# Optimization experiments

Hardware: AMD Instinct MI355X
Metric: run time of the kernel (lower is better)

## Reference

```python
import jax, jax.numpy as jnp
import numpy as np

NUM_EXPERTS = 8


def setup_inputs() -> dict:
    key = jax.random.key(0)
    k1, k2, k3, k4 = jax.random.split(key, 4)
    d_model, d_ff, E = 768, 3072, NUM_EXPERTS
    B, S = 4, 1024
    scale_in = 1.0 / np.sqrt(d_model)
    scale_ff = 1.0 / np.sqrt(d_ff)
    return {
        "hidden_states": jax.random.normal(k1, (B, S, d_model), dtype=jnp.float32),
        "router_weight": jax.random.normal(k2, (d_model, E), dtype=jnp.float32) * scale_in,
        "wi": jax.random.normal(k3, (E, d_model, d_ff), dtype=jnp.float32) * scale_in,
        "wo": jax.random.normal(k4, (E, d_ff, d_model), dtype=jnp.float32) * scale_ff,
    }


def reference(hidden_states, router_weight, wi, wo):
    # --- Top-1 router (HF computes softmax in fp32) ---
    router_logits = jnp.einsum("bsd,de->bse", hidden_states.astype(jnp.float32), router_weight.astype(jnp.float32))  # [B,S,E]
    probs = jax.nn.softmax(router_logits, axis=-1)
    expert_index = jnp.argmax(probs, axis=-1)                      # [B,S] int
    router_mask = jax.nn.one_hot(expert_index, NUM_EXPERTS, dtype=probs.dtype)  # [B,S,E]
    router_probs = jnp.max(probs, axis=-1, keepdims=True).astype(hidden_states.dtype)  # [B,S,1]

    # --- Experts: dense per-expert MLP, combined by the one-hot top-1 mask.
    # Every token is routed to exactly one expert, so masked-sum == dispatch/combine.
    h = jax.nn.relu(jnp.einsum("bsd,edf->bsef", hidden_states, wi))  # [B,S,E,d_ff]
    y = jnp.einsum("bsef,efd->bsed", h, wo)                           # [B,S,E,d_model]
    next_states = jnp.einsum("bse,bsed->bsd", router_mask.astype(hidden_states.dtype), y)

    out = router_probs * next_states
    return out, router_logits, expert_index
```

## Files before the change

### kernel.cpp

```cpp
#include <hip/hip_runtime.h>


typedef __attribute__((ext_vector_type(4))) float f32x4;
typedef __attribute__((ext_vector_type(8))) short short8;
typedef unsigned short ushort_t;
typedef unsigned int uint32;

#define DEVFN static __device__ __forceinline__
#define MFMA __builtin_amdgcn_mfma_f32_16x16x32_bf16

constexpr int NTOK = 4096;
constexpr int DM   = 768;
constexpr int DF   = 3072;
constexpr int NE   = 8;
constexpr int TM   = 128;
constexpr int MAXTILES = NTOK / TM + NE;
constexpr int MAXR  = MAXTILES * TM;
constexpr int BK    = 32;
constexpr int KS2   = 2;
constexpr int BSTR  = 40;

DEVFN ushort_t f2bf(float f) {
  uint32 u = __float_as_uint(f);
  u += 0x7fffu + ((u >> 16) & 1u);
  return (ushort_t)(u >> 16);
}
DEVFN float bf2f(ushort_t u) { return __uint_as_float((uint32)u << 16); }
DEVFN uint32 pkbf(float a, float b) {
  return (__float_as_uint(b) & 0xffff0000u) | (__float_as_uint(a) >> 16);
}

DEVFN void gl16(const void* g, void* l) {
  __builtin_amdgcn_global_load_lds(
      (const __attribute__((address_space(1))) void*)g,
      (__attribute__((address_space(3))) void*)l, 16, 0, 0);
}

__global__ __launch_bounds__(256) void k_router(
    const float* __restrict__ X, const float* __restrict__ Wr,
    float* __restrict__ out_logits, float* __restrict__ out_idx,
    int* __restrict__ expert_of, float* __restrict__ prob) {
  int wid = threadIdx.x >> 6, lane = threadIdx.x & 63;
  int t = blockIdx.x * 4 + wid;
  const float* xrow = X + (size_t)t * DM;
  double acc[NE];
#pragma unroll
  for (int e = 0; e < NE; e++) acc[e] = 0.0;
  for (int d0 = 0; d0 < DM; d0 += 64) {
    int d = d0 + lane;
    float x = xrow[d];
    const float4* w4 = (const float4*)(Wr + (size_t)d * NE);
    float4 wa = w4[0], wb = w4[1];
    acc[0] += (double)x * wa.x; acc[1] += (double)x * wa.y;
    acc[2] += (double)x * wa.z; acc[3] += (double)x * wa.w;
    acc[4] += (double)x * wb.x; acc[5] += (double)x * wb.y;
    acc[6] += (double)x * wb.z; acc[7] += (double)x * wb.w;
  }
#pragma unroll
  for (int e = 0; e < NE; e++) {
#pragma unroll
    for (int s = 32; s > 0; s >>= 1) acc[e] += __shfl_xor(acc[e], s);
  }
#pragma unroll
  for (int e = 0; e < NE; e++)
    if (lane == e) out_logits[(size_t)t * NE + e] = (float)acc[e];
  double m = acc[0]; int idx = 0;
#pragma unroll
  for (int e = 1; e < NE; e++) if (acc[e] > m) { m = acc[e]; idx = e; }
  float s = 0.f;
#pragma unroll
  for (int e = 0; e < NE; e++) s += expf((float)(acc[e] - m));
  if (lane == 0) {
    out_idx[t] = (float)idx;
    expert_of[t] = idx;
    prob[t] = 1.f / s;
  }
}

__global__ __launch_bounds__(64) void k_scan(
    const int* __restrict__ expert_of, const float* __restrict__ prob,
    int* __restrict__ meta, int* __restrict__ perm,
    float* __restrict__ prob_g) {
  __shared__ int exl[NTOK];
  int lane = threadIdx.x;
  const int4* src = (const int4*)expert_of;
  int4* dst = (int4*)exl;
#pragma unroll
  for (int j = 0; j < NTOK / 4 / 64; j++) dst[j * 64 + lane] = src[j * 64 + lane];
  __syncthreads();
  int cnt[NE];
#pragma unroll
  for (int e = 0; e < NE; e++) cnt[e] = 0;
  for (int j = 0; j < 64; j++) {
    int ex = exl[lane * 64 + j];
#pragma unroll
    for (int e = 0; e < NE; e++) cnt[e] += (ex == e);
  }
  int base[NE], tot[NE];
#pragma unroll
  for (int e = 0; e < NE; e++) {
    int inc = cnt[e];
#pragma unroll
    for (int s = 1; s < 64; s <<= 1) {
      int o = __shfl_up(inc, s);
      if (lane >= s) inc += o;
    }
    base[e] = inc - cnt[e];
    tot[e] = __shfl(inc, 63);
  }
  int segStart[NE];
  int pos = 0, nt = 0;
#pragma unroll
  for (int e = 0; e < NE; e++) {
    segStart[e] = pos;
    int tiles = (tot[e] + TM - 1) / TM;
    if (lane == 0) {
      meta[8 + e] = pos;
      meta[16 + e] = pos + tot[e];
      for (int i = 0; i < tiles; i++) {
        meta[64 + nt + i] = e;
        meta[128 + nt + i] = pos + i * TM;
      }
    }
    nt += tiles;
    pos += tiles * TM;
  }
  if (lane == 0) meta[24] = nt;
  int cum[NE];
#pragma unroll
  for (int e = 0; e < NE; e++) cum[e] = segStart[e] + base[e];
  for (int j = 0; j < 64; j++) {
    int t = lane * 64 + j;
    int ex = exl[lane * 64 + j];
    int p = 0;
#pragma unroll
    for (int e = 0; e < NE; e++) p += (ex == e) ? cum[e] : 0;
#pragma unroll
    for (int e = 0; e < NE; e++) cum[e] += (ex == e);
    perm[p] = t;
    prob_g[p] = prob[t];
  }
}

__global__ __launch_bounds__(256) void k_copy(
    const float* __restrict__ X, const int* __restrict__ meta,
    const int* __restrict__ perm, ushort_t* __restrict__ Xg) {
  int bt = blockIdx.y;
  if (bt >= meta[24]) return;
  int e = meta[64 + bt], row0 = meta[128 + bt], segEnd = meta[16 + e];
  int wid = threadIdx.x >> 6, lane = threadIdx.x & 63;
  int r = row0 + blockIdx.x * 4 + wid;
  if (r >= segEnd) return;
  int tok = perm[r];
  const float2* s2 = (const float2*)(X + (size_t)tok * DM);
  uint32* d2 = (uint32*)(Xg + (size_t)r * DM);
#pragma unroll
  for (int i = 0; i < DM / 128; i++) {
    float2 v = s2[i * 64 + lane];
    d2[i * 64 + lane] = (uint32)f2bf(v.x) | ((uint32)f2bf(v.y) << 16);
  }
}

template <int KTOT, int NB, int KSPLIT, bool FIRST>
__global__ __launch_bounds__(256, 3) void k_gemm8(
    const ushort_t* __restrict__ A, const float* __restrict__ Bw,
    const int* __restrict__ meta, ushort_t* __restrict__ Obf) {
  constexpr int NKTT = KTOT / KSPLIT / BK;
  __shared__ short A_lds[2][128 * BK];
  __shared__ short B_lds[2][128 * BSTR];

  int bt = blockIdx.y;
  if (bt >= meta[24]) return;
  int e    = meta[64 + bt];
  int row0 = meta[128 + bt];
  int n0, koff, z;
  if constexpr (FIRST) {
    n0 = blockIdx.x * 128; koff = 0; z = 0;
  } else {
    n0 = (blockIdx.x / KSPLIT) * 128; z = blockIdx.x % KSPLIT;
    koff = z * (KTOT / KSPLIT);
  }

  int tid = threadIdx.x, lane = tid & 63, w = tid >> 6;
  int wr = w >> 1, wc = w & 1;

  int srcSlot = (lane & 3) ^ ((lane >> 3) & 3);
  const ushort_t* aS = A + (size_t)(row0 + (tid >> 2)) * KTOT + koff + srcSlot * 8;
  int dstOff = w * 512;

#define STAGE_A(buf, kt)                                                      \
  do {                                                                        \
    gl16(aS + (size_t)(kt) * BK, &A_lds[buf][dstOff]);                        \
    gl16(aS + (size_t)(kt) * BK + (size_t)64 * KTOT,                          \
         &A_lds[buf][dstOff + 2048]);                                         \
  } while (0)

  int kq = tid >> 5, nb = tid & 31;
  const float* bS = Bw + (size_t)e * KTOT * NB + ((size_t)koff + kq * 4) * NB
                    + n0 + nb * 4;
  float4 bv0, bv1, bv2, bv3;

#define LOAD_B(kt)                                                            \
  do {                                                                        \
    const float* b0 = bS + (size_t)(kt) * BK * NB;                            \
    bv0 = *(const float4*)(b0);                                               \
    bv1 = *(const float4*)(b0 + NB);                                          \
    bv2 = *(const float4*)(b0 + 2 * NB);                                      \
    bv3 = *(const float4*)(b0 + 3 * NB);                                      \
  } while (0)

#define WRITE_B(buf)                                                          \
  do {                                                                        \
    _Pragma("unroll") for (int nn = 0; nn < 4; nn++) {                        \
      int n = nb * 4 + nn;                                                    \
      uint32 w0 = pkbf(((const float*)&bv0)[nn], ((const float*)&bv1)[nn]);   \
      uint32 w1 = pkbf(((const float*)&bv2)[nn], ((const float*)&bv3)[nn]);   \
      uint2* wp = (uint2*)&B_lds[buf][n * BSTR + ((kq ^ (n & 6)) << 2)];      \
      *wp = (uint2){w0, w1};                                                  \
    }                                                                         \
  } while (0)

  int kslotRd = ((lane >> 4) ^ ((lane >> 1) & 3)) * 8;
  int aOff[4], bOff[4];
#pragma unroll
  for (int m = 0; m < 4; m++)
    aOff[m] = (wr * 64 + m * 16 + (lane & 15)) * BK + kslotRd;
#pragma unroll
  for (int n = 0; n < 4; n++) {
    int col = wc * 64 + n * 16 + (lane & 15);
    bOff[n] = col * BSTR + (((lane >> 4) * 2) ^ (col & 6)) * 4;
  }

  f32x4 acc[4][4];
#pragma unroll
  for (int m = 0; m < 4; m++)
#pragma unroll
    for (int n = 0; n < 4; n++) acc[m][n] = (f32x4){0.f, 0.f, 0.f, 0.f};

  LOAD_B(0);
  STAGE_A(0, 0);
  WRITE_B(0);
  __syncthreads();

#pragma unroll 2
  for (int t = 0; t < NKTT; ++t) {
    int cur = t & 1;
    if (t + 1 < NKTT) {
      LOAD_B(t + 1);
      STAGE_A(cur ^ 1, t + 1);
    }
    const short* aB = A_lds[cur];
    const short* bB = B_lds[cur];
    short8 af[4], bf[4];
#pragma unroll
    for (int m = 0; m < 4; m++) af[m] = *(const short8*)&aB[aOff[m]];
#pragma unroll
    for (int n = 0; n < 4; n++) bf[n] = *(const short8*)&bB[bOff[n]];
    __builtin_amdgcn_s_setprio(1);
#pragma unroll
    for (int m = 0; m < 4; m++)
#pragma unroll
      for (int n = 0; n < 4; n++)
        acc[m][n] = MFMA(af[m], bf[n], acc[m][n], 0, 0, 0);
    __builtin_amdgcn_s_setprio(0);
    if (t + 1 < NKTT) WRITE_B(cur ^ 1);
    __syncthreads();
  }
#undef STAGE_A
#undef LOAD_B
#undef WRITE_B

  ushort_t* dst = FIRST ? Obf : Obf + (size_t)z * MAXR * NB;
#pragma unroll
  for (int m = 0; m < 4; m++) {
    int rowb = row0 + wr * 64 + m * 16 + (lane >> 4) * 4;
#pragma unroll
    for (int n = 0; n < 4; n++) {
      int col = n0 + wc * 64 + n * 16 + (lane & 15);
#pragma unroll
      for (int r = 0; r < 4; r++) {
        float v = acc[m][n][r];
        if (FIRST) v = v > 0.f ? v : 0.f;
        dst[(size_t)(rowb + r) * NB + col] = f2bf(v);
      }
    }
  }
}

__global__ __launch_bounds__(256) void k_reduce(
    const ushort_t* __restrict__ P, const int* __restrict__ meta,
    const int* __restrict__ perm, const float* __restrict__ prob_g,
    float* __restrict__ out) {
  int bt = blockIdx.y;
  if (bt >= meta[24]) return;
  int e = meta[64 + bt], row0 = meta[128 + bt], segEnd = meta[16 + e];
  int c0 = blockIdx.x * 64;
  int t = threadIdx.x;
  int col = c0 + (t & 7) * 8;
#pragma unroll
  for (int i = 0; i < 4; i++) {
    int r = row0 + (t >> 3) + i * 32;
    if (r >= segEnd) continue;
    int tok = perm[r];
    float p = prob_g[r];
    float s[8];
#pragma unroll
    for (int j = 0; j < 8; j++) s[j] = 0.f;
#pragma unroll
    for (int z = 0; z < KS2; z++) {
      short8 v = *(const short8*)&P[((size_t)z * MAXR + r) * DM + col];
#pragma unroll
      for (int j = 0; j < 8; j++) s[j] += bf2f((ushort_t)v[j]);
    }
    float4 o0 = {p * s[0], p * s[1], p * s[2], p * s[3]};
    float4 o1 = {p * s[4], p * s[5], p * s[6], p * s[7]};
    *(float4*)&out[(size_t)tok * DM + col] = o0;
    *(float4*)&out[(size_t)tok * DM + col + 4] = o1;
  }
}

extern "C" void kernel_launch(void* const* d_in, const int* in_sizes, int n_in,
                              void* d_out, int out_size, void* d_ws, size_t ws_size,
                              hipStream_t stream) {
  const float* X  = (const float*)d_in[0];
  const float* Wr = (const float*)d_in[1];
  const float* wi = (const float*)d_in[2];
  const float* wo = (const float*)d_in[3];

  float* out        = (float*)d_out;
  float* out_logits = out + (size_t)NTOK * DM;
  float* out_idx    = out_logits + (size_t)NTOK * NE;

  char* w = (char*)d_ws;
  int*      meta      = (int*)w;
  int*      expert_of = (int*)(w + 4096);
  float*    prob      = (float*)(w + 20480);
  int*      perm      = (int*)(w + 36864);
  float*    prob_g    = (float*)(w + 61440);
  ushort_t* Xg        = (ushort_t*)(w + 131072);
  ushort_t* H         = Xg + (size_t)MAXR * DM;
  ushort_t* P         = H + (size_t)MAXR * DF;

  k_router<<<NTOK / 4, 256, 0, stream>>>(X, Wr, out_logits, out_idx,
                                         expert_of, prob);
  k_scan<<<1, 64, 0, stream>>>(expert_of, prob, meta, perm, prob_g);
  k_copy<<<dim3(TM / 4, MAXTILES), 256, 0, stream>>>(X, meta, perm, Xg);
  k_gemm8<DM, DF, 1, true><<<dim3(DF / 128, MAXTILES), 256, 0, stream>>>(
      Xg, wi, meta, H);
  k_gemm8<DF, DM, KS2, false><<<dim3((DM / 128) * KS2, MAXTILES), 256, 0, stream>>>(
      H, wo, meta, P);
  k_reduce<<<dim3(DM / 64, MAXTILES), 256, 0, stream>>>(P, meta, perm, prob_g, out);
}
```

Measured before the change: 151.1 us.

## Double GEMM row tile to 256, raise split-K to 4, rework B LDS swizzle

Expert token tiles grow from 128 to 256 rows, so each workgroup computes 256x128 with 8x4 MFMA accumulators per wave. This halves how often each expert's weight tile is reloaded and converted. The second GEMM's split-K goes from 2 to 4 to keep enough workgroups, and the reduce kernel is updated to match. B loads become coalesced scalar column loads stored in an XOR-swizzled, unpadded LDS layout. The trade-offs are more padding waste per expert, higher register pressure under a 3-waves launch bound, and more partial-sum traffic in the reduce step.

```diff
diff --git a/kernel.cpp b/kernel.cpp
--- a/kernel.cpp
+++ b/kernel.cpp
@@ -13,12 +13,11 @@
 constexpr int DM   = 768;
 constexpr int DF   = 3072;
 constexpr int NE   = 8;
-constexpr int TM   = 128;
+constexpr int TM   = 256;
 constexpr int MAXTILES = NTOK / TM + NE;
 constexpr int MAXR  = MAXTILES * TM;
 constexpr int BK    = 32;
-constexpr int KS2   = 2;
-constexpr int BSTR  = 40;
+constexpr int KS    = 4;
 
 DEVFN ushort_t f2bf(float f) {
   uint32 u = __float_as_uint(f);
@@ -166,8 +165,8 @@
     const ushort_t* __restrict__ A, const float* __restrict__ Bw,
     const int* __restrict__ meta, ushort_t* __restrict__ Obf) {
   constexpr int NKTT = KTOT / KSPLIT / BK;
-  __shared__ short A_lds[2][128 * BK];
-  __shared__ short B_lds[2][128 * BSTR];
+  __shared__ short A_lds[2][256 * BK];
+  __shared__ short B_lds[2][128 * BK];
 
   int bt = blockIdx.y;
   if (bt >= meta[24]) return;
@@ -190,50 +189,54 @@
 
 #define STAGE_A(buf, kt)                                                      \
   do {                                                                        \
-    gl16(aS + (size_t)(kt) * BK, &A_lds[buf][dstOff]);                        \
-    gl16(aS + (size_t)(kt) * BK + (size_t)64 * KTOT,                          \
-         &A_lds[buf][dstOff + 2048]);                                         \
+    const ushort_t* a0 = aS + (size_t)(kt) * BK;                              \
+    gl16(a0,                        &A_lds[buf][dstOff]);                     \
+    gl16(a0 + (size_t)64 * KTOT,    &A_lds[buf][dstOff + 2048]);              \
+    gl16(a0 + (size_t)128 * KTOT,   &A_lds[buf][dstOff + 4096]);              \
+    gl16(a0 + (size_t)192 * KTOT,   &A_lds[buf][dstOff + 6144]);              \
   } while (0)
 
-  int kq = tid >> 5, nb = tid & 31;
+  int kq = tid >> 5, nc = tid & 31;
   const float* bS = Bw + (size_t)e * KTOT * NB + ((size_t)koff + kq * 4) * NB
-                    + n0 + nb * 4;
-  float4 bv0, bv1, bv2, bv3;
+                    + n0 + nc;
+  float bv[4][4];
 
 #define LOAD_B(kt)                                                            \
   do {                                                                        \
     const float* b0 = bS + (size_t)(kt) * BK * NB;                            \
-    bv0 = *(const float4*)(b0);                                               \
-    bv1 = *(const float4*)(b0 + NB);                                          \
-    bv2 = *(const float4*)(b0 + 2 * NB);                                      \
-    bv3 = *(const float4*)(b0 + 3 * NB);                                      \
+    _Pragma("unroll") for (int kk = 0; kk < 4; kk++)                          \
+      _Pragma("unroll") for (int nn = 0; nn < 4; nn++)                        \
+        bv[kk][nn] = b0[(size_t)kk * NB + nn * 32];                           \
   } while (0)
 
 #define WRITE_B(buf)                                                          \
   do {                                                                        \
     _Pragma("unroll") for (int nn = 0; nn < 4; nn++) {                        \
-      int n = nb * 4 + nn;                                                    \
-      uint32 w0 = pkbf(((const float*)&bv0)[nn], ((const float*)&bv1)[nn]);   \
-      uint32 w1 = pkbf(((const float*)&bv2)[nn], ((const float*)&bv3)[nn]);   \
-      uint2* wp = (uint2*)&B_lds[buf][n * BSTR + ((kq ^ (n & 6)) << 2)];      \
-      *wp = (uint2){w0, w1};                                                  \
+      int c = nc + 32 * nn;                                                   \
+      int sg = (c ^ (c >> 2)) & 3;                                            \
+      int ad = c * BK + (((kq >> 1) ^ sg) << 3) + ((kq & 1) << 2);            \
+      uint32 w0 = pkbf(bv[0][nn], bv[1][nn]);                                 \
+      uint32 w1 = pkbf(bv[2][nn], bv[3][nn]);                                 \
+      *(uint2*)&B_lds[buf][ad] = (uint2){w0, w1};                             \
     }                                                                         \
   } while (0)
 
-  int kslotRd = ((lane >> 4) ^ ((lane >> 1) & 3)) * 8;
-  int aOff[4], bOff[4];
-#pragma unroll
-  for (int m = 0; m < 4; m++)
-    aOff[m] = (wr * 64 + m * 16 + (lane & 15)) * BK + kslotRd;
+  int g = lane >> 4;
+  int kslotRd = (g ^ ((lane >> 1) & 3)) * 8;
+  int aOff[8], bOff[4];
+#pragma unroll
+  for (int m = 0; m < 8; m++)
+    aOff[m] = (wr * 128 + m * 16 + (lane & 15)) * BK + kslotRd;
 #pragma unroll
   for (int n = 0; n < 4; n++) {
     int col = wc * 64 + n * 16 + (lane & 15);
-    bOff[n] = col * BSTR + (((lane >> 4) * 2) ^ (col & 6)) * 4;
-  }
-
-  f32x4 acc[4][4];
-#pragma unroll
-  for (int m = 0; m < 4; m++)
+    int sg = (col ^ (col >> 2)) & 3;
+    bOff[n] = col * BK + ((g ^ sg) << 3);
+  }
+
+  f32x4 acc[8][4];
+#pragma unroll
+  for (int m = 0; m < 8; m++)
 #pragma unroll
     for (int n = 0; n < 4; n++) acc[m][n] = (f32x4){0.f, 0.f, 0.f, 0.f};
 
@@ -251,14 +254,14 @@
     }
     const short* aB = A_lds[cur];
     const short* bB = B_lds[cur];
-    short8 af[4], bf[4];
-#pragma unroll
-    for (int m = 0; m < 4; m++) af[m] = *(const short8*)&aB[aOff[m]];
+    short8 af[8], bf[4];
+#pragma unroll
+    for (int m = 0; m < 8; m++) af[m] = *(const short8*)&aB[aOff[m]];
 #pragma unroll
     for (int n = 0; n < 4; n++) bf[n] = *(const short8*)&bB[bOff[n]];
     __builtin_amdgcn_s_setprio(1);
 #pragma unroll
-    for (int m = 0; m < 4; m++)
+    for (int m = 0; m < 8; m++)
 #pragma unroll
       for (int n = 0; n < 4; n++)
         acc[m][n] = MFMA(af[m], bf[n], acc[m][n], 0, 0, 0);
@@ -272,8 +275,8 @@
 
   ushort_t* dst = FIRST ? Obf : Obf + (size_t)z * MAXR * NB;
 #pragma unroll
-  for (int m = 0; m < 4; m++) {
-    int rowb = row0 + wr * 64 + m * 16 + (lane >> 4) * 4;
+  for (int m = 0; m < 8; m++) {
+    int rowb = row0 + wr * 128 + m * 16 + (lane >> 4) * 4;
 #pragma unroll
     for (int n = 0; n < 4; n++) {
       int col = n0 + wc * 64 + n * 16 + (lane & 15);
@@ -298,7 +301,7 @@
   int t = threadIdx.x;
   int col = c0 + (t & 7) * 8;
 #pragma unroll
-  for (int i = 0; i < 4; i++) {
+  for (int i = 0; i < 8; i++) {
     int r = row0 + (t >> 3) + i * 32;
     if (r >= segEnd) continue;
     int tok = perm[r];
@@ -307,7 +310,7 @@
 #pragma unroll
     for (int j = 0; j < 8; j++) s[j] = 0.f;
 #pragma unroll
-    for (int z = 0; z < KS2; z++) {
+    for (int z = 0; z < KS; z++) {
       short8 v = *(const short8*)&P[((size_t)z * MAXR + r) * DM + col];
 #pragma unroll
       for (int j = 0; j < 8; j++) s[j] += bf2f((ushort_t)v[j]);
@@ -347,7 +350,7 @@
   k_copy<<<dim3(TM / 4, MAXTILES), 256, 0, stream>>>(X, meta, perm, Xg);
   k_gemm8<DM, DF, 1, true><<<dim3(DF / 128, MAXTILES), 256, 0, stream>>>(
       Xg, wi, meta, H);
-  k_gemm8<DF, DM, KS2, false><<<dim3((DM / 128) * KS2, MAXTILES), 256, 0, stream>>>(
+  k_gemm8<DF, DM, KS, false><<<dim3((DM / 128) * KS, MAXTILES), 256, 0, stream>>>(
       H, wo, meta, P);
   k_reduce<<<dim3(DM / 64, MAXTILES), 256, 0, stream>>>(P, meta, perm, prob_g, out);
 }
```

Measured after the change: 378.2 us. +150.3%, slower.
